# Optimization experiments

Hardware: AMD Instinct MI355X
Metric: run time of the kernel (lower is better)

## Reference

```python
import jax, jax.numpy as jnp
import numpy as np

N = 50000
E = 800000
IN_C, HID_C, OUT_C = 128, 256, 128
BN_EPS = 1e-5


def glorot(key, shape):
    fan_in, fan_out = shape
    lim = float(np.sqrt(6.0 / (fan_in + fan_out)))
    return jax.random.uniform(key, shape, jnp.float32, -lim, lim)


def setup_inputs() -> dict:
    key = jax.random.key(0)
    ks = jax.random.split(key, 16)
    inp = {
        "x": jax.random.normal(ks[0], (N, IN_C), jnp.float32),
        "edge_index": jax.random.randint(ks[1], (2, E), 0, N, jnp.int64),
        # SAGEConv 1 (in->hid): lin_l has bias, lin_r has no bias (PyG default)
        "wl1": glorot(ks[2], (IN_C, HID_C)), "bl1": jnp.zeros((HID_C,), jnp.float32),
        "wr1": glorot(ks[3], (IN_C, HID_C)),
        # SAGEConv 2 (hid->hid)
        "wl2": glorot(ks[4], (HID_C, HID_C)), "bl2": jnp.zeros((HID_C,), jnp.float32),
        "wr2": glorot(ks[5], (HID_C, HID_C)),
        # SAGEConv 3 (hid->out)
        "wl3": glorot(ks[6], (HID_C, OUT_C)), "bl3": jnp.zeros((OUT_C,), jnp.float32),
        "wr3": glorot(ks[7], (HID_C, OUT_C)),
        # BatchNorm params (eval mode: running stats)
        "bn1_w": jnp.ones((HID_C,), jnp.float32), "bn1_b": jnp.zeros((HID_C,), jnp.float32),
        "bn1_m": jax.random.normal(ks[8], (HID_C,), jnp.float32) * 0.1,
        "bn1_v": jax.random.uniform(ks[9], (HID_C,), jnp.float32, 0.5, 1.5),
        "bn2_w": jnp.ones((HID_C,), jnp.float32), "bn2_b": jnp.zeros((HID_C,), jnp.float32),
        "bn2_m": jax.random.normal(ks[10], (HID_C,), jnp.float32) * 0.1,
        "bn2_v": jax.random.uniform(ks[11], (HID_C,), jnp.float32, 0.5, 1.5),
    }
    return inp


def sage_conv(x, src, dst, wl, bl, wr):
    # mean aggregation of source-node features at destination nodes
    agg = jax.ops.segment_sum(x[src], dst, num_segments=N)          # [N, d_in]
    deg = jax.ops.segment_sum(jnp.ones((E,), x.dtype), dst, num_segments=N)
    mean = agg / jnp.maximum(deg, 1.0)[:, None]
    return mean @ wl + bl + x @ wr                                   # [N, d_out]


def batch_norm(x, w, b, m, v):
    return (x - m) * jax.lax.rsqrt(v + BN_EPS) * w + b


def reference(x, edge_index, wl1, bl1, wr1, wl2, bl2, wr2, wl3, bl3, wr3,
              bn1_w, bn1_b, bn1_m, bn1_v, bn2_w, bn2_b, bn2_m, bn2_v):
    src, dst = edge_index[0], edge_index[1]
    # layer 1: SAGEConv -> BN -> ReLU (dropout is identity in eval mode)
    h = sage_conv(x, src, dst, wl1, bl1, wr1)
    h = jax.nn.relu(batch_norm(h, bn1_w, bn1_b, bn1_m, bn1_v))
    # layer 2
    h = sage_conv(h, src, dst, wl2, bl2, wr2)
    h = jax.nn.relu(batch_norm(h, bn2_w, bn2_b, bn2_m, bn2_v))
    # output layer: plain SAGEConv
    return sage_conv(h, src, dst, wl3, bl3, wr3)
```

## Files before the change

kernel.cpp:

```cpp
#include <hip/hip_runtime.h>
#include <hip/hip_bf16.h>

#define NN 50000
#define NE 800000
#define NSB 49
#define AGG_BLOCKS 2048

typedef __attribute__((ext_vector_type(8))) short bh8;
typedef __attribute__((ext_vector_type(4))) float f32x4;

static __device__ __forceinline__ unsigned short f2bf(float f){
  unsigned u = __float_as_uint(f);
  unsigned r = (u + 0x7fffu + ((u >> 16) & 1u)) >> 16;
  return (unsigned short)r;
}
static __device__ __forceinline__ float bflo(unsigned u){ return __uint_as_float(u << 16); }
static __device__ __forceinline__ float bfhi(unsigned u){ return __uint_as_float(u & 0xffff0000u); }
static __device__ __forceinline__ unsigned packbf2(float lo, float hi){
  return ((unsigned)f2bf(hi) << 16) | (unsigned)f2bf(lo);
}
static __device__ __forceinline__ unsigned char f2fp8(float v){
  return (unsigned char)(__builtin_amdgcn_cvt_pk_fp8_f32(v, v, 0, false) & 0xff);
}

static __device__ __forceinline__ void gload16(const void* g, void* l){
  __builtin_amdgcn_global_load_lds(
      (const __attribute__((address_space(1))) unsigned int*)g,
      (__attribute__((address_space(3))) unsigned int*)l, 16, 0, 0);
}

__global__ void hist_k(const int* __restrict__ dstv, int* __restrict__ cnt,
                       int* __restrict__ rank){
  int i = blockIdx.x * 256 + threadIdx.x;
  if (i < NE) rank[i] = atomicAdd(&cnt[dstv[i]], 1);
}

__global__ __launch_bounds__(256) void scan1_k(const int* __restrict__ cnt,
                                               int* __restrict__ rowp,
                                               int* __restrict__ bsum){
  __shared__ int sa[256], sb[256];
  const int t = threadIdx.x, blk = blockIdx.x;
  const int base = blk * 1024 + t * 4;
  int4 v = make_int4(0, 0, 0, 0);
  if (base + 3 < NN) v = *reinterpret_cast<const int4*>(cnt + base);
  else if (base < NN){
    v.x = cnt[base];
    if (base + 1 < NN) v.y = cnt[base + 1];
    if (base + 2 < NN) v.z = cnt[base + 2];
  }
  const int s = v.x + v.y + v.z + v.w;
  sa[t] = s; __syncthreads();
  int* a = sa; int* b = sb;
  for (int off = 1; off < 256; off <<= 1){
    int val = a[t]; if (t >= off) val += a[t - off];
    b[t] = val; __syncthreads();
    int* tmp = a; a = b; b = tmp;
  }
  const int ex = a[t] - s;
  if (base < NN){
    rowp[base] = ex;
    if (base + 1 < NN) rowp[base + 1] = ex + v.x;
    if (base + 2 < NN) rowp[base + 2] = ex + v.x + v.y;
    if (base + 3 < NN) rowp[base + 3] = ex + v.x + v.y + v.z;
  }
  if (t == 255) bsum[blk] = a[255];
}

__global__ void scan2_k(int* __restrict__ bsum){
  __shared__ int s[64];
  const int t = threadIdx.x;
  s[t] = (t < NSB) ? bsum[t] : 0;
  __syncthreads();
  if (t == 0){
    int run = 0;
    for (int i = 0; i < NSB; ++i){ int c = s[i]; s[i] = run; run += c; }
  }
  __syncthreads();
  if (t < NSB) bsum[t] = s[t];
}

__global__ __launch_bounds__(256) void scan3_k(int* __restrict__ rowp,
                                               const int* __restrict__ bsum){
  const int blk = blockIdx.x;
  const int base = blk * 1024 + threadIdx.x * 4;
  const int off = bsum[blk];
  #pragma unroll
  for (int i = 0; i < 4; ++i){
    int idx = base + i;
    if (idx < NN) rowp[idx] += off;
  }
  if (blk == 0 && threadIdx.x == 0) rowp[NN] = NE;
}

__global__ __launch_bounds__(256) void fill_k(const int* __restrict__ srcv,
                       const int* __restrict__ dstv,
                       const int* __restrict__ rank,
                       const int* __restrict__ rowp, int* __restrict__ csrc){
  const int part  = blockIdx.x & 7;
  const int chunk = blockIdx.x >> 3;
  const int lo = part * (NN / 8);
  const int hi = lo + (NN / 8);
  const int base = chunk * (NE / 128);
  const int endi = base + (NE / 128);
  for (int i = base + threadIdx.x; i < endi; i += 256){
    int d = dstv[i];
    if (d >= lo && d < hi){
      csrc[rowp[d] + rank[i]] = srcv[i];
    }
  }
}

__global__ void f2b_k(const float4* __restrict__ x, uint2* __restrict__ xb,
                      unsigned* __restrict__ xq){
  int i = blockIdx.x * 256 + threadIdx.x;
  if (i < NN * 128 / 4){
    float4 v = x[i];
    uint2 o; o.x = packbf2(v.x, v.y); o.y = packbf2(v.z, v.w);
    xb[i] = o;
    int w = 0;
    w = __builtin_amdgcn_cvt_pk_fp8_f32(v.x, v.y, w, false);
    w = __builtin_amdgcn_cvt_pk_fp8_f32(v.z, v.w, w, true);
    xq[i] = (unsigned)w;
  }
}

__global__ void prep_k(const float* __restrict__ wl1, const float* __restrict__ wr1,
                       const float* __restrict__ wl2, const float* __restrict__ wr2,
                       const float* __restrict__ wl3, const float* __restrict__ wr3,
                       const float* __restrict__ bl1, const float* __restrict__ bl2,
                       const float* __restrict__ bn1w, const float* __restrict__ bn1b,
                       const float* __restrict__ bn1m, const float* __restrict__ bn1v,
                       const float* __restrict__ bn2w, const float* __restrict__ bn2b,
                       const float* __restrict__ bn2m, const float* __restrict__ bn2v,
                       unsigned short* __restrict__ B1t, unsigned short* __restrict__ B2t,
                       unsigned short* __restrict__ B3t,
                       float* __restrict__ S1, float* __restrict__ T1,
                       float* __restrict__ S2, float* __restrict__ T2){
  int i = blockIdx.x * 256 + threadIdx.x;
  if (i < 65536){
    int n = i >> 8, k = i & 255;
    float v = (k < 128) ? wl1[k * 256 + n] : wr1[(k - 128) * 256 + n];
    B1t[n * 256 + k] = f2bf(v);
  } else if (i < 65536 + 131072){
    int j = i - 65536; int n = j >> 9, k = j & 511;
    float v = (k < 256) ? wl2[k * 256 + n] : wr2[(k - 256) * 256 + n];
    B2t[n * 512 + k] = f2bf(v);
  } else if (i < 65536 + 131072 + 65536){
    int j = i - (65536 + 131072); int n = j >> 8, k = j & 255;
    float v = (n < 128) ? wl3[k * 128 + n] : wr3[k * 128 + (n - 128)];
    B3t[n * 256 + k] = f2bf(v);
  } else if (i < 65536 + 131072 + 65536 + 512){
    int j = i - (65536 + 131072 + 65536);
    if (j < 256){
      float s = bn1w[j] * rsqrtf(bn1v[j] + 1e-5f);
      S1[j] = s; T1[j] = (bl1[j] - bn1m[j]) * s + bn1b[j];
    } else {
      int c = j - 256;
      float s = bn2w[c] * rsqrtf(bn2v[c] + 1e-5f);
      S2[c] = s; T2[c] = (bl2[c] - bn2m[c]) * s + bn2b[c];
    }
  }
}

__global__ __launch_bounds__(256) void agg128q_k(const unsigned short* __restrict__ featq,
                         unsigned* __restrict__ out,
                         const int* __restrict__ rowp, const int* __restrict__ csrc){
  const int lane = threadIdx.x & 63;
  const int node0 = __builtin_amdgcn_readfirstlane(blockIdx.x * 4 + (threadIdx.x >> 6));
  const int nw = gridDim.x * 4;
  for (int node = node0; node < NN; node += nw){
    const int start = rowp[node], end = rowp[node + 1];
    float a0 = 0.f, a1 = 0.f, b0 = 0.f, b1 = 0.f;
    int e = start;
    for (; e + 7 < end; e += 8){
      unsigned u0 = featq[(size_t)csrc[e]     * 64 + lane];
      unsigned u1 = featq[(size_t)csrc[e + 1] * 64 + lane];
      unsigned u2 = featq[(size_t)csrc[e + 2] * 64 + lane];
      unsigned u3 = featq[(size_t)csrc[e + 3] * 64 + lane];
      unsigned u4 = featq[(size_t)csrc[e + 4] * 64 + lane];
      unsigned u5 = featq[(size_t)csrc[e + 5] * 64 + lane];
      unsigned u6 = featq[(size_t)csrc[e + 6] * 64 + lane];
      unsigned u7 = featq[(size_t)csrc[e + 7] * 64 + lane];
      a0 += __builtin_amdgcn_cvt_f32_fp8(u0, 0); a1 += __builtin_amdgcn_cvt_f32_fp8(u0, 1);
      b0 += __builtin_amdgcn_cvt_f32_fp8(u1, 0); b1 += __builtin_amdgcn_cvt_f32_fp8(u1, 1);
      a0 += __builtin_amdgcn_cvt_f32_fp8(u2, 0); a1 += __builtin_amdgcn_cvt_f32_fp8(u2, 1);
      b0 += __builtin_amdgcn_cvt_f32_fp8(u3, 0); b1 += __builtin_amdgcn_cvt_f32_fp8(u3, 1);
      a0 += __builtin_amdgcn_cvt_f32_fp8(u4, 0); a1 += __builtin_amdgcn_cvt_f32_fp8(u4, 1);
      b0 += __builtin_amdgcn_cvt_f32_fp8(u5, 0); b1 += __builtin_amdgcn_cvt_f32_fp8(u5, 1);
      a0 += __builtin_amdgcn_cvt_f32_fp8(u6, 0); a1 += __builtin_amdgcn_cvt_f32_fp8(u6, 1);
      b0 += __builtin_amdgcn_cvt_f32_fp8(u7, 0); b1 += __builtin_amdgcn_cvt_f32_fp8(u7, 1);
    }
    for (; e < end; ++e){
      unsigned u = featq[(size_t)csrc[e] * 64 + lane];
      a0 += __builtin_amdgcn_cvt_f32_fp8(u, 0); a1 += __builtin_amdgcn_cvt_f32_fp8(u, 1);
    }
    int d = end - start;
    float inv = 1.f / (float)(d > 0 ? d : 1);
    out[(size_t)node * 64 + lane] = packbf2((a0 + b0) * inv, (a1 + b1) * inv);
  }
}

#define DEC8(u, x0, x1, x2, x3) { \
  x0 += __builtin_amdgcn_cvt_f32_fp8((u), 0); \
  x1 += __builtin_amdgcn_cvt_f32_fp8((u), 1); \
  x2 += __builtin_amdgcn_cvt_f32_fp8((u), 2); \
  x3 += __builtin_amdgcn_cvt_f32_fp8((u), 3); }

__global__ __launch_bounds__(256) void agg256q_k(const unsigned* __restrict__ featq, unsigned* __restrict__ out,
                         const int* __restrict__ rowp, const int* __restrict__ csrc){
  const int lane = threadIdx.x & 63;
  const int node0 = __builtin_amdgcn_readfirstlane(blockIdx.x * 4 + (threadIdx.x >> 6));
  const int nw = gridDim.x * 4;
  for (int node = node0; node < NN; node += nw){
    const int start = rowp[node], end = rowp[node + 1];
    float a0 = 0.f, a1 = 0.f, a2 = 0.f, a3 = 0.f;
    float b0 = 0.f, b1 = 0.f, b2 = 0.f, b3 = 0.f;
    int e = start;
    for (; e + 7 < end; e += 8){
      unsigned u0 = featq[(size_t)csrc[e]     * 64 + lane];
      unsigned u1 = featq[(size_t)csrc[e + 1] * 64 + lane];
      unsigned u2 = featq[(size_t)csrc[e + 2] * 64 + lane];
      unsigned u3 = featq[(size_t)csrc[e + 3] * 64 + lane];
      unsigned u4 = featq[(size_t)csrc[e + 4] * 64 + lane];
      unsigned u5 = featq[(size_t)csrc[e + 5] * 64 + lane];
      unsigned u6 = featq[(size_t)csrc[e + 6] * 64 + lane];
      unsigned u7 = featq[(size_t)csrc[e + 7] * 64 + lane];
      DEC8(u0, a0, a1, a2, a3) DEC8(u1, b0, b1, b2, b3)
      DEC8(u2, a0, a1, a2, a3) DEC8(u3, b0, b1, b2, b3)
      DEC8(u4, a0, a1, a2, a3) DEC8(u5, b0, b1, b2, b3)
      DEC8(u6, a0, a1, a2, a3) DEC8(u7, b0, b1, b2, b3)
    }
    for (; e < end; ++e){
      unsigned u = featq[(size_t)csrc[e] * 64 + lane];
      DEC8(u, a0, a1, a2, a3)
    }
    int d = end - start;
    float inv = 1.f / (float)(d > 0 ? d : 1);
    uint2 o; o.x = packbf2((a0 + b0) * inv, (a1 + b1) * inv);
    o.y = packbf2((a2 + b2) * inv, (a3 + b3) * inv);
    *reinterpret_cast<uint2*>(out + (size_t)node * 128 + lane * 2) = o;
  }
}

__global__ __launch_bounds__(256) void final_k(const unsigned short* __restrict__ tq, float* __restrict__ out,
                        const int* __restrict__ rowp, const int* __restrict__ csrc,
                        const float* __restrict__ bl3){
  const int lane = threadIdx.x & 63;
  const int node0 = __builtin_amdgcn_readfirstlane(blockIdx.x * 4 + (threadIdx.x >> 6));
  const int nw = gridDim.x * 4;
  for (int node = node0; node < NN; node += nw){
    const int start = rowp[node], end = rowp[node + 1];
    float a0 = 0.f, a1 = 0.f, b0 = 0.f, b1 = 0.f;
    int e = start;
    for (; e + 7 < end; e += 8){
      unsigned u0 = tq[(size_t)csrc[e]     * 64 + lane];
      unsigned u1 = tq[(size_t)csrc[e + 1] * 64 + lane];
      unsigned u2 = tq[(size_t)csrc[e + 2] * 64 + lane];
      unsigned u3 = tq[(size_t)csrc[e + 3] * 64 + lane];
      unsigned u4 = tq[(size_t)csrc[e + 4] * 64 + lane];
      unsigned u5 = tq[(size_t)csrc[e + 5] * 64 + lane];
      unsigned u6 = tq[(size_t)csrc[e + 6] * 64 + lane];
      unsigned u7 = tq[(size_t)csrc[e + 7] * 64 + lane];
      a0 += __builtin_amdgcn_cvt_f32_fp8(u0, 0); a1 += __builtin_amdgcn_cvt_f32_fp8(u0, 1);
      b0 += __builtin_amdgcn_cvt_f32_fp8(u1, 0); b1 += __builtin_amdgcn_cvt_f32_fp8(u1, 1);
      a0 += __builtin_amdgcn_cvt_f32_fp8(u2, 0); a1 += __builtin_amdgcn_cvt_f32_fp8(u2, 1);
      b0 += __builtin_amdgcn_cvt_f32_fp8(u3, 0); b1 += __builtin_amdgcn_cvt_f32_fp8(u3, 1);
      a0 += __builtin_amdgcn_cvt_f32_fp8(u4, 0); a1 += __builtin_amdgcn_cvt_f32_fp8(u4, 1);
      b0 += __builtin_amdgcn_cvt_f32_fp8(u5, 0); b1 += __builtin_amdgcn_cvt_f32_fp8(u5, 1);
      a0 += __builtin_amdgcn_cvt_f32_fp8(u6, 0); a1 += __builtin_amdgcn_cvt_f32_fp8(u6, 1);
      b0 += __builtin_amdgcn_cvt_f32_fp8(u7, 0); b1 += __builtin_amdgcn_cvt_f32_fp8(u7, 1);
    }
    for (; e < end; ++e){
      unsigned u = tq[(size_t)csrc[e] * 64 + lane];
      a0 += __builtin_amdgcn_cvt_f32_fp8(u, 0); a1 += __builtin_amdgcn_cvt_f32_fp8(u, 1);
    }
    int d = end - start;
    float inv = 1.f / (float)(d > 0 ? d : 1);
    float2* o = reinterpret_cast<float2*>(out + (size_t)node * 128) + lane;
    float2 v = *o;
    v.x += (a0 + b0) * inv + bl3[lane * 2];
    v.y += (a1 + b1) * inv + bl3[lane * 2 + 1];
    *o = v;
  }
}

template<int KTOT, int K0, int MODE>
__global__ __launch_bounds__(256) void gemm_k(
    const unsigned short* __restrict__ A0, const unsigned short* __restrict__ A1,
    const unsigned short* __restrict__ Bt,
    const float* __restrict__ S, const float* __restrict__ Tt,
    unsigned short* __restrict__ outB, unsigned char* __restrict__ outQ,
    float* __restrict__ outF, int M)
{
  __shared__ __align__(16) unsigned char lds[49152];
  const int tid = threadIdx.x;
  const int lane = tid & 63;
  const int wv = tid >> 6;
  const int wm = wv >> 1, wn = wv & 1;

  const int nwg = gridDim.x;
  const int q = nwg >> 3, r8 = nwg & 7;
  const int xcd = blockIdx.x & 7, idx = blockIdx.x >> 3;
  const int wg = (xcd < r8) ? xcd * (q + 1) + idx : r8 * (q + 1) + (xcd - r8) * q + idx;
  const int bm = wg >> 1, bn = wg & 1;

  const int rr0 = tid >> 2,         g0 = (tid & 3) ^ ((tid >> 3) & 3);
  const int rr1 = (tid + 256) >> 2, g1 = ((tid + 256) & 3) ^ (((tid + 256) >> 3) & 3);
  int growA0 = bm * 128 + rr0; if (growA0 > M - 1) growA0 = M - 1;
  int growA1 = bm * 128 + rr1; if (growA1 > M - 1) growA1 = M - 1;
  const size_t browA0 = (size_t)(bn * 128 + rr0) * KTOT;
  const size_t browA1 = (size_t)(bn * 128 + rr1) * KTOT;

  const int l15 = lane & 15, kg = lane >> 4;
  const int slot = (kg ^ ((l15 >> 1) & 3)) * 16;

  constexpr int NT = KTOT / 32;

  auto STAGE = [&](int buf, int kt){
    const int kb = kt * 32;
    const unsigned short* Ap; int pitch, kk;
    if (KTOT == K0 || kb < K0){ Ap = A0; pitch = K0; kk = kb; }
    else { Ap = A1; pitch = KTOT - K0; kk = kb - K0; }
    unsigned char* base = lds + buf * 16384;
    gload16(Ap + (size_t)growA0 * pitch + kk + g0 * 8, base + tid * 16);
    gload16(Ap + (size_t)growA1 * pitch + kk + g1 * 8, base + 4096 + tid * 16);
    gload16(Bt + browA0 + kb + g0 * 8, base + 8192 + tid * 16);
    gload16(Bt + browA1 + kb + g1 * 8, base + 12288 + tid * 16);
  };

  f32x4 acc[4][4];
  #pragma unroll
  for (int i = 0; i < 4; ++i)
    #pragma unroll
    for (int j = 0; j < 4; ++j){ acc[i][j][0]=0.f; acc[i][j][1]=0.f; acc[i][j][2]=0.f; acc[i][j][3]=0.f; }

  STAGE(0, 0);
  if (NT > 1) STAGE(1, 1);

  int rb = 0, sb = 2;
  for (int kt = 0; kt < NT; ++kt){
    if (kt < NT - 1) asm volatile("s_waitcnt vmcnt(4)" ::: "memory");
    else             asm volatile("s_waitcnt vmcnt(0)" ::: "memory");
    __builtin_amdgcn_s_barrier();
    __builtin_amdgcn_sched_barrier(0);

    if (kt + 2 < NT){ STAGE(sb, kt + 2); sb = (sb == 2) ? 0 : sb + 1; }

    unsigned char* base = lds + rb * 16384;
    rb = (rb == 2) ? 0 : rb + 1;

    bh8 af[4], bf[4];
    #pragma unroll
    for (int mi = 0; mi < 4; ++mi){
      int rA = wm * 64 + mi * 16 + l15;
      af[mi] = *reinterpret_cast<const bh8*>(base + rA * 64 + slot);
    }
    #pragma unroll
    for (int ni = 0; ni < 4; ++ni){
      int rB = wn * 64 + ni * 16 + l15;
      bf[ni] = *reinterpret_cast<const bh8*>(base + 8192 + rB * 64 + slot);
    }
    __builtin_amdgcn_s_setprio(1);
    #pragma unroll
    for (int mi = 0; mi < 4; ++mi)
      #pragma unroll
      for (int ni = 0; ni < 4; ++ni)
        acc[mi][ni] = __builtin_amdgcn_mfma_f32_16x16x32_bf16(af[mi], bf[ni], acc[mi][ni], 0, 0, 0);
    __builtin_amdgcn_s_setprio(0);
  }

  #pragma unroll
  for (int mi = 0; mi < 4; ++mi){
    int rbase = bm * 128 + wm * 64 + mi * 16 + ((lane >> 4) << 2);
    #pragma unroll
    for (int ni = 0; ni < 4; ++ni){
      int col = bn * 128 + wn * 64 + ni * 16 + (lane & 15);
      #pragma unroll
      for (int j = 0; j < 4; ++j){
        int row = rbase + j;
        if (row < M){
          float v = acc[mi][ni][j];
          if (MODE == 0){
            v = v * S[col] + Tt[col];
            v = v > 0.f ? v : 0.f;
            outB[(size_t)row * 256 + col] = f2bf(v);
            if (outQ) outQ[(size_t)row * 256 + col] = f2fp8(v);
          } else {
            if (col < 128) outQ[(size_t)row * 128 + col] = f2fp8(v);
            else           outF[(size_t)row * 128 + (col - 128)] = v;
          }
        }
      }
    }
  }
}

__global__ __launch_bounds__(256) void gemm23_k(
    const unsigned short* __restrict__ A0 ,
    const unsigned short* __restrict__ A1 ,
    const unsigned short* __restrict__ B2 ,
    const unsigned short* __restrict__ B3 ,
    const float* __restrict__ S, const float* __restrict__ Tt,
    unsigned char* __restrict__ tq, float* __restrict__ outF, int M)
{
  __shared__ __align__(16) unsigned char lds[61440];
  const int tid = threadIdx.x;
  const int lane = tid & 63;
  const int wv = tid >> 6;

  const int nwg = gridDim.x;
  const int q = nwg >> 3, r8 = nwg & 7;
  const int xcd = blockIdx.x & 7, idx = blockIdx.x >> 3;
  const int bm = (xcd < r8) ? xcd * (q + 1) + idx : r8 * (q + 1) + (xcd - r8) * q + idx;

  const int l15 = lane & 15, kg = lane >> 4;
  const int slot = (kg ^ ((l15 >> 1) & 3)) * 16;
  const int rr = tid >> 2;
  const int g  = (tid & 3) ^ ((tid >> 3) & 3);
  int grow = bm * 64 + rr; if (grow > M - 1) grow = M - 1;

  auto STAGE = [&](int buf, int kt){
    const int kb = kt * 32;
    const unsigned short* Ap = (kb < 256) ? A0 : A1;
    const int kk = (kb < 256) ? kb : kb - 256;
    unsigned char* base = lds + buf * 20480;
    gload16(Ap + (size_t)grow * 256 + kk + g * 8, base + tid * 16);
    gload16(B2 + (size_t)(rr      ) * 512 + kb + g * 8, base +  4096 + tid * 16);
    gload16(B2 + (size_t)(rr +  64) * 512 + kb + g * 8, base +  8192 + tid * 16);
    gload16(B2 + (size_t)(rr + 128) * 512 + kb + g * 8, base + 12288 + tid * 16);
    gload16(B2 + (size_t)(rr + 192) * 512 + kb + g * 8, base + 16384 + tid * 16);
  };

  f32x4 acc[4][4];
  #pragma unroll
  for (int i = 0; i < 4; ++i)
    #pragma unroll
    for (int j = 0; j < 4; ++j){ acc[i][j][0]=0.f; acc[i][j][1]=0.f; acc[i][j][2]=0.f; acc[i][j][3]=0.f; }

  STAGE(0, 0);
  STAGE(1, 1);

  int rb = 0, sb = 2;
  #pragma unroll 1
  for (int kt = 0; kt < 16; ++kt){
    if (kt < 15) asm volatile("s_waitcnt vmcnt(5)" ::: "memory");
    else         asm volatile("s_waitcnt vmcnt(0)" ::: "memory");
    __builtin_amdgcn_s_barrier();
    __builtin_amdgcn_sched_barrier(0);

    if (kt + 2 < 16){ STAGE(sb, kt + 2); sb = (sb == 2) ? 0 : sb + 1; }

    unsigned char* base = lds + rb * 20480;
    rb = (rb == 2) ? 0 : rb + 1;

    bh8 af[4], bf[4];
    #pragma unroll
    for (int mi = 0; mi < 4; ++mi)
      af[mi] = *reinterpret_cast<const bh8*>(base + (mi * 16 + l15) * 64 + slot);
    #pragma unroll
    for (int ni = 0; ni < 4; ++ni)
      bf[ni] = *reinterpret_cast<const bh8*>(base + 4096 + (wv * 64 + ni * 16 + l15) * 64 + slot);

    __builtin_amdgcn_s_setprio(1);
    #pragma unroll
    for (int mi = 0; mi < 4; ++mi)
      #pragma unroll
      for (int ni = 0; ni < 4; ++ni)
        acc[mi][ni] = __builtin_amdgcn_mfma_f32_16x16x32_bf16(bf[ni], af[mi], acc[mi][ni], 0, 0, 0);
    __builtin_amdgcn_s_setprio(0);
  }

  __syncthreads();
  #pragma unroll
  for (int mi = 0; mi < 4; ++mi){
    const int row = mi * 16 + l15;
    #pragma unroll
    for (int ni = 0; ni < 4; ++ni){
      const int c0 = wv * 64 + ni * 16 + kg * 4;
      float v0 = acc[mi][ni][0] * S[c0]     + Tt[c0];     v0 = v0 > 0.f ? v0 : 0.f;
      float v1 = acc[mi][ni][1] * S[c0 + 1] + Tt[c0 + 1]; v1 = v1 > 0.f ? v1 : 0.f;
      float v2 = acc[mi][ni][2] * S[c0 + 2] + Tt[c0 + 2]; v2 = v2 > 0.f ? v2 : 0.f;
      float v3 = acc[mi][ni][3] * S[c0 + 3] + Tt[c0 + 3]; v3 = v3 > 0.f ? v3 : 0.f;
      uint2 w; w.x = packbf2(v0, v1); w.y = packbf2(v2, v3);
      const int chunk = wv * 8 + ni * 2 + (kg >> 1);
      const int byte = row * 512 + ((chunk ^ (row & 7)) * 16) + (kg & 1) * 8;
      *reinterpret_cast<uint2*>(lds + byte) = w;
    }
  }
  __syncthreads();

  f32x4 acc2[4][4];
  #pragma unroll
  for (int i = 0; i < 4; ++i)
    #pragma unroll
    for (int j = 0; j < 4; ++j){ acc2[i][j][0]=0.f; acc2[i][j][1]=0.f; acc2[i][j][2]=0.f; acc2[i][j][3]=0.f; }

  #pragma unroll 1
  for (int kt = 0; kt < 8; ++kt){
    const int kb = kt * 32;
    bh8 af2[4], bf2[4];
    #pragma unroll
    for (int mi = 0; mi < 4; ++mi){
      const int row = mi * 16 + l15;
      const int chunk = kt * 4 + kg;
      af2[mi] = *reinterpret_cast<const bh8*>(lds + row * 512 + ((chunk ^ (row & 7)) * 16));
    }
    #pragma unroll
    for (int ni = 0; ni < 4; ++ni)
      bf2[ni] = *reinterpret_cast<const bh8*>(B3 + (size_t)(wv * 64 + ni * 16 + l15) * 256 + kb + kg * 8);
    __builtin_amdgcn_s_setprio(1);
    #pragma unroll
    for (int mi = 0; mi < 4; ++mi)
      #pragma unroll
      for (int ni = 0; ni < 4; ++ni)
        acc2[mi][ni] = __builtin_amdgcn_mfma_f32_16x16x32_bf16(af2[mi], bf2[ni], acc2[mi][ni], 0, 0, 0);
    __builtin_amdgcn_s_setprio(0);
  }

  #pragma unroll
  for (int mi = 0; mi < 4; ++mi){
    const int rbase = bm * 64 + mi * 16 + (kg << 2);
    #pragma unroll
    for (int ni = 0; ni < 4; ++ni){
      const int col = wv * 64 + ni * 16 + l15;
      #pragma unroll
      for (int j = 0; j < 4; ++j){
        const int row = rbase + j;
        if (row < M){
          float v = acc2[mi][ni][j];
          if (col < 128) tq[(size_t)row * 128 + col] = f2fp8(v);
          else           outF[(size_t)row * 128 + (col - 128)] = v;
        }
      }
    }
  }
}

extern "C" void kernel_launch(void* const* d_in, const int* in_sizes, int n_in,
                              void* d_out, int out_size, void* d_ws, size_t ws_size,
                              hipStream_t stream) {
  (void)in_sizes; (void)n_in; (void)out_size; (void)ws_size;
  const float* x   = (const float*)d_in[0];
  const int*   ei  = (const int*)d_in[1];
  const int*   srcv = ei;
  const int*   dstv = ei + NE;
  const float* wl1 = (const float*)d_in[2];
  const float* bl1 = (const float*)d_in[3];
  const float* wr1 = (const float*)d_in[4];
  const float* wl2 = (const float*)d_in[5];
  const float* bl2 = (const float*)d_in[6];
  const float* wr2 = (const float*)d_in[7];
  const float* wl3 = (const float*)d_in[8];
  const float* bl3 = (const float*)d_in[9];
  const float* wr3 = (const float*)d_in[10];
  const float* bn1w = (const float*)d_in[11];
  const float* bn1b = (const float*)d_in[12];
  const float* bn1m = (const float*)d_in[13];
  const float* bn1v = (const float*)d_in[14];
  const float* bn2w = (const float*)d_in[15];
  const float* bn2b = (const float*)d_in[16];
  const float* bn2m = (const float*)d_in[17];
  const float* bn2v = (const float*)d_in[18];

  char* ws = (char*)d_ws;
  size_t off = 0;
  auto alloc = [&](size_t bytes) -> void* {
    void* p = ws + off;
    off += (bytes + 255) & ~(size_t)255;
    return p;
  };
  int* cnt  = (int*)alloc((size_t)NN * 4);
  int* rank = (int*)alloc((size_t)NE * 4);
  int* rowp = (int*)alloc((size_t)(NN + 1) * 4);
  int* csrc = (int*)alloc((size_t)NE * 4);
  int* bsum = (int*)alloc((size_t)NSB * 4);
  unsigned short* B1t = (unsigned short*)alloc(256 * 256 * 2);
  unsigned short* B2t = (unsigned short*)alloc(256 * 512 * 2);
  unsigned short* B3t = (unsigned short*)alloc(256 * 256 * 2);
  float* S1 = (float*)alloc(256 * 4);
  float* T1 = (float*)alloc(256 * 4);
  float* S2 = (float*)alloc(256 * 4);
  float* T2 = (float*)alloc(256 * 4);
  unsigned short* xb   = (unsigned short*)alloc((size_t)NN * 128 * 2);
  unsigned short* agg1 = (unsigned short*)alloc((size_t)NN * 128 * 2);
  unsigned short* h1   = (unsigned short*)alloc((size_t)NN * 256 * 2);
  unsigned short* h2   = (unsigned short*)alloc((size_t)NN * 256 * 2);
  unsigned short* agg2 = xb;
  unsigned char*  h1q  = (unsigned char*)h2;
  unsigned*       xq   = (unsigned*)((unsigned char*)h2 + (size_t)NN * 256);
  unsigned char*  tq   = (unsigned char*)h2;
  float* outp = (float*)d_out;

  hipMemsetAsync(cnt, 0, (size_t)NN * 4, stream);
  hist_k<<<(NE + 255) / 256, 256, 0, stream>>>(dstv, cnt, rank);
  scan1_k<<<NSB, 256, 0, stream>>>(cnt, rowp, bsum);
  scan2_k<<<1, 64, 0, stream>>>(bsum);
  scan3_k<<<NSB, 256, 0, stream>>>(rowp, bsum);
  fill_k<<<1024, 256, 0, stream>>>(srcv, dstv, rank, rowp, csrc);
  prep_k<<<1026, 256, 0, stream>>>(wl1, wr1, wl2, wr2, wl3, wr3, bl1, bl2,
                                   bn1w, bn1b, bn1m, bn1v, bn2w, bn2b, bn2m, bn2v,
                                   B1t, B2t, B3t, S1, T1, S2, T2);
  f2b_k<<<(NN * 128 / 4 + 255) / 256, 256, 0, stream>>>((const float4*)x, (uint2*)xb, xq);

  agg128q_k<<<AGG_BLOCKS, 256, 0, stream>>>((const unsigned short*)xq, (unsigned*)agg1, rowp, csrc);
  gemm_k<256, 128, 0><<<782, 256, 0, stream>>>(agg1, xb, B1t, S1, T1, h1, h1q, nullptr, NN);
  agg256q_k<<<AGG_BLOCKS, 256, 0, stream>>>((const unsigned*)h1q, (unsigned*)agg2, rowp, csrc);
  gemm23_k<<<782, 256, 0, stream>>>(agg2, h1, B2t, B3t, S2, T2, tq, outp, NN);
  final_k<<<AGG_BLOCKS, 256, 0, stream>>>((const unsigned short*)tq, outp, rowp, csrc, bl3);
}
```

Baseline: 242.0 us.

## Stage full-K A tile in LDS once, stream weights directly from global

Both GEMM kernels drop the triple-buffered per-K-step LDS pipeline for A and B. Each block now loads its whole 64-row A tile (all of K) into swizzled LDS in one pass, then reads B fragments straight from global/L2 inside a fully unrolled K loop. The layer-1 GEMM also changes from 128x128 tiles to 64x256 row-block tiles with a fused BN/ReLU epilogue. This removes per-step barriers and repeated B staging, but global B loads now sit on the MFMA critical path, and the larger LDS footprint may lower occupancy.

Result: slower. 267.0 us (+10.4%).

```diff
diff --git a/kernel.cpp b/kernel.cpp
--- a/kernel.cpp
+++ b/kernel.cpp
@@ -284,111 +284,91 @@
   }
 }
 
-template<int KTOT, int K0, int MODE>
-__global__ __launch_bounds__(256) void gemm_k(
+template<int KTOT, int K0>
+__global__ __launch_bounds__(256) void gemmA_k(
     const unsigned short* __restrict__ A0, const unsigned short* __restrict__ A1,
     const unsigned short* __restrict__ Bt,
     const float* __restrict__ S, const float* __restrict__ Tt,
-    unsigned short* __restrict__ outB, unsigned char* __restrict__ outQ,
-    float* __restrict__ outF, int M)
+    unsigned short* __restrict__ outB, unsigned char* __restrict__ outQ, int M)
 {
-  __shared__ __align__(16) unsigned char lds[49152];
+  constexpr int CB = KTOT * 2;
+  constexpr int NC = CB / 16;
+  constexpr int NB = K0 / 8;
+  constexpr int RPR = 4096 / CB;
+  constexpr int NRND = 64 / RPR;
+  __shared__ __align__(16) unsigned char lds[64 * CB];
+
   const int tid = threadIdx.x;
   const int lane = tid & 63;
   const int wv = tid >> 6;
-  const int wm = wv >> 1, wn = wv & 1;
 
   const int nwg = gridDim.x;
   const int q = nwg >> 3, r8 = nwg & 7;
   const int xcd = blockIdx.x & 7, idx = blockIdx.x >> 3;
-  const int wg = (xcd < r8) ? xcd * (q + 1) + idx : r8 * (q + 1) + (xcd - r8) * q + idx;
-  const int bm = wg >> 1, bn = wg & 1;
-
-  const int rr0 = tid >> 2,         g0 = (tid & 3) ^ ((tid >> 3) & 3);
-  const int rr1 = (tid + 256) >> 2, g1 = ((tid + 256) & 3) ^ (((tid + 256) >> 3) & 3);
-  int growA0 = bm * 128 + rr0; if (growA0 > M - 1) growA0 = M - 1;
-  int growA1 = bm * 128 + rr1; if (growA1 > M - 1) growA1 = M - 1;
-  const size_t browA0 = (size_t)(bn * 128 + rr0) * KTOT;
-  const size_t browA1 = (size_t)(bn * 128 + rr1) * KTOT;
+  const int bm = (xcd < r8) ? xcd * (q + 1) + idx : r8 * (q + 1) + (xcd - r8) * q + idx;
 
   const int l15 = lane & 15, kg = lane >> 4;
-  const int slot = (kg ^ ((l15 >> 1) & 3)) * 16;
-
-  constexpr int NT = KTOT / 32;
-
-  auto STAGE = [&](int buf, int kt){
+
+  {
+    const int rr = tid / NC;
+    const int ch = tid % NC;
+    #pragma unroll
+    for (int j = 0; j < NRND; ++j){
+      const int row = j * RPR + rr;
+      const int s = ch ^ (row & 7);
+      int grow = bm * 64 + row; if (grow > M - 1) grow = M - 1;
+      const unsigned short* src;
+      if (KTOT == K0 || s < NB) src = A0 + (size_t)grow * K0 + s * 8;
+      else                      src = A1 + (size_t)grow * (KTOT - K0) + (s - NB) * 8;
+      gload16(src, lds + j * 4096 + tid * 16);
+    }
+  }
+  asm volatile("s_waitcnt vmcnt(0)" ::: "memory");
+  __builtin_amdgcn_s_barrier();
+
+  f32x4 acc[4][4];
+  #pragma unroll
+  for (int i = 0; i < 4; ++i)
+    #pragma unroll
+    for (int j = 0; j < 4; ++j){ acc[i][j][0]=0.f; acc[i][j][1]=0.f; acc[i][j][2]=0.f; acc[i][j][3]=0.f; }
+
+  #pragma unroll
+  for (int kt = 0; kt < KTOT / 32; ++kt){
     const int kb = kt * 32;
-    const unsigned short* Ap; int pitch, kk;
-    if (KTOT == K0 || kb < K0){ Ap = A0; pitch = K0; kk = kb; }
-    else { Ap = A1; pitch = KTOT - K0; kk = kb - K0; }
-    unsigned char* base = lds + buf * 16384;
-    gload16(Ap + (size_t)growA0 * pitch + kk + g0 * 8, base + tid * 16);
-    gload16(Ap + (size_t)growA1 * pitch + kk + g1 * 8, base + 4096 + tid * 16);
-    gload16(Bt + browA0 + kb + g0 * 8, base + 8192 + tid * 16);
-    gload16(Bt + browA1 + kb + g1 * 8, base + 12288 + tid * 16);
-  };
-
-  f32x4 acc[4][4];
-  #pragma unroll
-  for (int i = 0; i < 4; ++i)
-    #pragma unroll
-    for (int j = 0; j < 4; ++j){ acc[i][j][0]=0.f; acc[i][j][1]=0.f; acc[i][j][2]=0.f; acc[i][j][3]=0.f; }
-
-  STAGE(0, 0);
-  if (NT > 1) STAGE(1, 1);
-
-  int rb = 0, sb = 2;
-  for (int kt = 0; kt < NT; ++kt){
-    if (kt < NT - 1) asm volatile("s_waitcnt vmcnt(4)" ::: "memory");
-    else             asm volatile("s_waitcnt vmcnt(0)" ::: "memory");
-    __builtin_amdgcn_s_barrier();
-    __builtin_amdgcn_sched_barrier(0);
-
-    if (kt + 2 < NT){ STAGE(sb, kt + 2); sb = (sb == 2) ? 0 : sb + 1; }
-
-    unsigned char* base = lds + rb * 16384;
-    rb = (rb == 2) ? 0 : rb + 1;
-
     bh8 af[4], bf[4];
     #pragma unroll
     for (int mi = 0; mi < 4; ++mi){
-      int rA = wm * 64 + mi * 16 + l15;
-      af[mi] = *reinterpret_cast<const bh8*>(base + rA * 64 + slot);
+      const int row = mi * 16 + l15;
+      const int c = kt * 4 + kg;
+      af[mi] = *reinterpret_cast<const bh8*>(lds + row * CB + ((c ^ (row & 7)) * 16));
     }
     #pragma unroll
     for (int ni = 0; ni < 4; ++ni){
-      int rB = wn * 64 + ni * 16 + l15;
-      bf[ni] = *reinterpret_cast<const bh8*>(base + 8192 + rB * 64 + slot);
-    }
-    __builtin_amdgcn_s_setprio(1);
+      const int col = wv * 64 + ni * 16 + l15;
+      bf[ni] = *reinterpret_cast<const bh8*>(Bt + (size_t)col * KTOT + kb + kg * 8);
+    }
     #pragma unroll
     for (int mi = 0; mi < 4; ++mi)
       #pragma unroll
       for (int ni = 0; ni < 4; ++ni)
         acc[mi][ni] = __builtin_amdgcn_mfma_f32_16x16x32_bf16(af[mi], bf[ni], acc[mi][ni], 0, 0, 0);
-    __builtin_amdgcn_s_setprio(0);
   }
 
   #pragma unroll
   for (int mi = 0; mi < 4; ++mi){
-    int rbase = bm * 128 + wm * 64 + mi * 16 + ((lane >> 4) << 2);
+    const int rbase = bm * 64 + mi * 16 + (kg << 2);
     #pragma unroll
     for (int ni = 0; ni < 4; ++ni){
-      int col = bn * 128 + wn * 64 + ni * 16 + (lane & 15);
+      const int col = wv * 64 + ni * 16 + l15;
       #pragma unroll
       for (int j = 0; j < 4; ++j){
-        int row = rbase + j;
+        const int row = rbase + j;
         if (row < M){
           float v = acc[mi][ni][j];
-          if (MODE == 0){
-            v = v * S[col] + Tt[col];
-            v = v > 0.f ? v : 0.f;
-            outB[(size_t)row * 256 + col] = f2bf(v);
-            if (outQ) outQ[(size_t)row * 256 + col] = f2fp8(v);
-          } else {
-            if (col < 128) outQ[(size_t)row * 128 + col] = f2fp8(v);
-            else           outF[(size_t)row * 128 + (col - 128)] = v;
-          }
+          v = v * S[col] + Tt[col];
+          v = v > 0.f ? v : 0.f;
+          outB[(size_t)row * 256 + col] = f2bf(v);
+          outQ[(size_t)row * 256 + col] = f2fp8(v);
         }
       }
     }
@@ -403,7 +383,7 @@
     const float* __restrict__ S, const float* __restrict__ Tt,
     unsigned char* __restrict__ tq, float* __restrict__ outF, int M)
 {
-  __shared__ __align__(16) unsigned char lds[61440];
+  __shared__ __align__(16) unsigned char lds[65536];
   const int tid = threadIdx.x;
   const int lane = tid & 63;
   const int wv = tid >> 6;
@@ -414,60 +394,49 @@
   const int bm = (xcd < r8) ? xcd * (q + 1) + idx : r8 * (q + 1) + (xcd - r8) * q + idx;
 
   const int l15 = lane & 15, kg = lane >> 4;
-  const int slot = (kg ^ ((l15 >> 1) & 3)) * 16;
-  const int rr = tid >> 2;
-  const int g  = (tid & 3) ^ ((tid >> 3) & 3);
-  int grow = bm * 64 + rr; if (grow > M - 1) grow = M - 1;
-
-  auto STAGE = [&](int buf, int kt){
+
+  {
+    const int rr = tid >> 6;
+    const int ch = tid & 63;
+    #pragma unroll
+    for (int j = 0; j < 16; ++j){
+      const int row = j * 4 + rr;
+      const int s = ch ^ (row & 7);
+      int grow = bm * 64 + row; if (grow > M - 1) grow = M - 1;
+      const unsigned short* src = (s < 32) ? (A0 + (size_t)grow * 256 + s * 8)
+                                           : (A1 + (size_t)grow * 256 + (s - 32) * 8);
+      gload16(src, lds + j * 4096 + tid * 16);
+    }
+  }
+  asm volatile("s_waitcnt vmcnt(0)" ::: "memory");
+  __builtin_amdgcn_s_barrier();
+
+  f32x4 acc[4][4];
+  #pragma unroll
+  for (int i = 0; i < 4; ++i)
+    #pragma unroll
+    for (int j = 0; j < 4; ++j){ acc[i][j][0]=0.f; acc[i][j][1]=0.f; acc[i][j][2]=0.f; acc[i][j][3]=0.f; }
+
+  #pragma unroll
+  for (int kt = 0; kt < 16; ++kt){
     const int kb = kt * 32;
-    const unsigned short* Ap = (kb < 256) ? A0 : A1;
-    const int kk = (kb < 256) ? kb : kb - 256;
-    unsigned char* base = lds + buf * 20480;
-    gload16(Ap + (size_t)grow * 256 + kk + g * 8, base + tid * 16);
-    gload16(B2 + (size_t)(rr      ) * 512 + kb + g * 8, base +  4096 + tid * 16);
-    gload16(B2 + (size_t)(rr +  64) * 512 + kb + g * 8, base +  8192 + tid * 16);
-    gload16(B2 + (size_t)(rr + 128) * 512 + kb + g * 8, base + 12288 + tid * 16);
-    gload16(B2 + (size_t)(rr + 192) * 512 + kb + g * 8, base + 16384 + tid * 16);
-  };
-
-  f32x4 acc[4][4];
-  #pragma unroll
-  for (int i = 0; i < 4; ++i)
-    #pragma unroll
-    for (int j = 0; j < 4; ++j){ acc[i][j][0]=0.f; acc[i][j][1]=0.f; acc[i][j][2]=0.f; acc[i][j][3]=0.f; }
-
-  STAGE(0, 0);
-  STAGE(1, 1);
-
-  int rb = 0, sb = 2;
-  #pragma unroll 1
-  for (int kt = 0; kt < 16; ++kt){
-    if (kt < 15) asm volatile("s_waitcnt vmcnt(5)" ::: "memory");
-    else         asm volatile("s_waitcnt vmcnt(0)" ::: "memory");
-    __builtin_amdgcn_s_barrier();
-    __builtin_amdgcn_sched_barrier(0);
-
-    if (kt + 2 < 16){ STAGE(sb, kt + 2); sb = (sb == 2) ? 0 : sb + 1; }
-
-    unsigned char* base = lds + rb * 20480;
-    rb = (rb == 2) ? 0 : rb + 1;
-
     bh8 af[4], bf[4];
     #pragma unroll
-    for (int mi = 0; mi < 4; ++mi)
-      af[mi] = *reinterpret_cast<const bh8*>(base + (mi * 16 + l15) * 64 + slot);
-    #pragma unroll
-    for (int ni = 0; ni < 4; ++ni)
-      bf[ni] = *reinterpret_cast<const bh8*>(base + 4096 + (wv * 64 + ni * 16 + l15) * 64 + slot);
-
-    __builtin_amdgcn_s_setprio(1);
+    for (int mi = 0; mi < 4; ++mi){
+      const int row = mi * 16 + l15;
+      const int c = kt * 4 + kg;
+      af[mi] = *reinterpret_cast<const bh8*>(lds + row * 1024 + ((c ^ (row & 7)) * 16));
+    }
+    #pragma unroll
+    for (int ni = 0; ni < 4; ++ni){
+      const int col = wv * 64 + ni * 16 + l15;
+      bf[ni] = *reinterpret_cast<const bh8*>(B2 + (size_t)col * 512 + kb + kg * 8);
+    }
     #pragma unroll
     for (int mi = 0; mi < 4; ++mi)
       #pragma unroll
       for (int ni = 0; ni < 4; ++ni)
         acc[mi][ni] = __builtin_amdgcn_mfma_f32_16x16x32_bf16(bf[ni], af[mi], acc[mi][ni], 0, 0, 0);
-    __builtin_amdgcn_s_setprio(0);
   }
 
   __syncthreads();
@@ -495,7 +464,7 @@
     #pragma unroll
     for (int j = 0; j < 4; ++j){ acc2[i][j][0]=0.f; acc2[i][j][1]=0.f; acc2[i][j][2]=0.f; acc2[i][j][3]=0.f; }
 
-  #pragma unroll 1
+  #pragma unroll
   for (int kt = 0; kt < 8; ++kt){
     const int kb = kt * 32;
     bh8 af2[4], bf2[4];
@@ -508,13 +477,11 @@
     #pragma unroll
     for (int ni = 0; ni < 4; ++ni)
       bf2[ni] = *reinterpret_cast<const bh8*>(B3 + (size_t)(wv * 64 + ni * 16 + l15) * 256 + kb + kg * 8);
-    __builtin_amdgcn_s_setprio(1);
     #pragma unroll
     for (int mi = 0; mi < 4; ++mi)
       #pragma unroll
       for (int ni = 0; ni < 4; ++ni)
         acc2[mi][ni] = __builtin_amdgcn_mfma_f32_16x16x32_bf16(af2[mi], bf2[ni], acc2[mi][ni], 0, 0, 0);
-    __builtin_amdgcn_s_setprio(0);
   }
 
   #pragma unroll
@@ -603,7 +570,7 @@
   f2b_k<<<(NN * 128 / 4 + 255) / 256, 256, 0, stream>>>((const float4*)x, (uint2*)xb, xq);
 
   agg128q_k<<<AGG_BLOCKS, 256, 0, stream>>>((const unsigned short*)xq, (unsigned*)agg1, rowp, csrc);
-  gemm_k<256, 128, 0><<<782, 256, 0, stream>>>(agg1, xb, B1t, S1, T1, h1, h1q, nullptr, NN);
+  gemmA_k<256, 128><<<782, 256, 0, stream>>>(agg1, xb, B1t, S1, T1, h1, h1q, NN);
   agg256q_k<<<AGG_BLOCKS, 256, 0, stream>>>((const unsigned*)h1q, (unsigned*)agg2, rowp, csrc);
   gemm23_k<<<782, 256, 0, stream>>>(agg2, h1, B2t, B3t, S2, T2, tq, outp, NN);
   final_k<<<AGG_BLOCKS, 256, 0, stream>>>((const unsigned short*)tq, outp, rowp, csrc, bl3);
```
